# Kernel optimization log

Hardware: AMD Instinct MI355X
Metric: run time of the kernel (lower is better)

Reference implementation:

```python
import jax, jax.numpy as jnp
import numpy as np

NUM_HEADS = 8
ROPE_THETA = 10.0


def _axial_angles(height, width, head_dim, theta):
    # frequencies: 1/theta^(arange(0, head_dim, 4)[:head_dim//4] / head_dim)  -> [head_dim//4]
    hd4 = head_dim // 4
    freqs = 1.0 / (theta ** (np.arange(0, head_dim, 4)[:hd4].astype(np.float32) / head_dim))
    t = np.arange(height * width)
    t_x = (t % width).astype(np.float32)
    t_y = (t // width).astype(np.float32)
    ang_x = np.outer(t_x, freqs)  # [n, head_dim//4]
    ang_y = np.outer(t_y, freqs)
    return jnp.asarray(ang_x), jnp.asarray(ang_y)


def _apply_rope(x, cos, sin):
    # x: [b, h, n, half]; cos/sin: [n, half//2]; complex-pair rotation on last dim
    xr = x[..., 0::2]
    xi = x[..., 1::2]
    out_r = xr * cos - xi * sin
    out_i = xr * sin + xi * cos
    return jnp.stack([out_r, out_i], axis=-1).reshape(x.shape)


def setup_inputs() -> dict:
    key = jax.random.key(0)
    ks = jax.random.split(key, 5)
    b, n, c = 4, 16384, 512
    x = jax.random.normal(ks[0], (b, n, c), dtype=jnp.float32)
    w_qkv = jax.random.normal(ks[1], (c, 3 * c), dtype=jnp.float32) * 0.02
    b_qkv = jax.random.normal(ks[2], (3 * c,), dtype=jnp.float32) * 0.02
    w_proj = jax.random.normal(ks[3], (c, c), dtype=jnp.float32) * 0.02
    b_proj = jax.random.normal(ks[4], (c,), dtype=jnp.float32) * 0.02
    return {"x": x, "w_qkv": w_qkv, "b_qkv": b_qkv, "w_proj": w_proj, "b_proj": b_proj,
            "height": 128, "width": 128}


def reference(x, w_qkv, b_qkv, w_proj, b_proj, height, width):
    b, n, c = x.shape
    h = NUM_HEADS
    hd = c // h
    half = hd // 2

    qkv = (x @ w_qkv + b_qkv).reshape(b, n, 3, h, hd).transpose(2, 0, 3, 1, 4)
    q, k, v = qkv[0], qkv[1], qkv[2]  # each [b, h, n, hd]

    ang_x, ang_y = _axial_angles(height, width, hd, ROPE_THETA)
    cx, sx = jnp.cos(ang_x), jnp.sin(ang_x)
    cy, sy = jnp.cos(ang_y), jnp.sin(ang_y)

    q = jnp.concatenate([_apply_rope(q[..., :half], cx, sx),
                         _apply_rope(q[..., half:], cy, sy)], axis=-1)
    k = jnp.concatenate([_apply_rope(k[..., :half], cx, sx),
                         _apply_rope(k[..., half:], cy, sy)], axis=-1)

    # kernel feature map: elu(x) + 1 (positive)
    q = jax.nn.elu(q) + 1.0
    k = jax.nn.elu(k) + 1.0

    # linear attention: O(n d^2)
    kv = jnp.einsum('bhnd,bhne->bhde', k, v)
    out = jnp.einsum('bhnd,bhde->bhne', q, kv)
    z = 1.0 / (jnp.einsum('bhnd,bhd->bhn', q, k.sum(axis=2)) + 1e-6)
    out = out * z[..., None]

    out = out.transpose(0, 2, 1, 3).reshape(b, n, c)
    return out @ w_proj + b_proj
```

## Files before the change

kernel.cpp:

```cpp
#include <hip/hip_runtime.h>
#include <math.h>

#define BATCH 4
#define NTOK  16384
#define CDIM  512
#define NH    8
#define HD    64
#define M_ROWS (BATCH*NTOK)
#define KDIM  512

typedef _Float16 f16;
typedef _Float16 f16x8 __attribute__((ext_vector_type(8)));
typedef _Float16 f16x4 __attribute__((ext_vector_type(4)));
typedef _Float16 f16x2 __attribute__((ext_vector_type(2)));
typedef float    f32x4 __attribute__((ext_vector_type(4)));

__device__ __forceinline__ void load_lds16(const void* g, void* l) {
    __builtin_amdgcn_global_load_lds(
        (const __attribute__((address_space(1))) void*)g,
        (__attribute__((address_space(3))) void*)l, 16, 0, 0);
}

__global__ void rope_tables(float* __restrict__ tab) {
    int tid = threadIdx.x;
    for (int i = 0; i < 16; i++) {
        int idx = tid + i * 256;
        int t   = (idx >> 4) & 127;
        int fi  = idx & 15;
        double freq = pow(10.0, -(double)fi / 16.0);
        double ang  = (double)t * freq;
        tab[idx * 2]     = (float)cos(ang);
        tab[idx * 2 + 1] = (float)sin(ang);
    }
}

__global__ void convert_x_f16(const float* __restrict__ in, f16* __restrict__ outp) {
    int i = blockIdx.x * 256 + threadIdx.x;
    float4 a = *(const float4*)&in[(size_t)i * 8];
    float4 b = *(const float4*)&in[(size_t)i * 8 + 4];
    f16x8 o;
    o[0]=(f16)a.x; o[1]=(f16)a.y; o[2]=(f16)a.z; o[3]=(f16)a.w;
    o[4]=(f16)b.x; o[5]=(f16)b.y; o[6]=(f16)b.z; o[7]=(f16)b.w;
    *(f16x8*)&outp[(size_t)i * 8] = o;
}

template<int PERM>
__global__ void convert_wT(const float* __restrict__ w, f16* __restrict__ wt, int N) {
    int idx = blockIdx.x * 256 + threadIdx.x;
    int n = idx >> 9, k = idx & 511;
    int tc = n;
    if (PERM) {
        int blk = n >> 5, pos = n & 31;
        tc = blk * 32 + ((pos < 16) ? (pos * 2) : ((pos - 16) * 2 + 1));
    }
    wt[idx] = (f16)w[(size_t)k * N + tc];
}

template<int MODE>
__global__ __launch_bounds__(256, 2)
void gemm_f16(const f16* __restrict__ A, const f16* __restrict__ Bt,
              const float* __restrict__ bias,
              float* __restrict__ Co,
              f16* __restrict__ qd, f16* __restrict__ kd, f16* __restrict__ vd,
              const float* __restrict__ tab, int ncol_tiles)
{
    __shared__ f16 As[128 * 64];
    __shared__ f16 Bs[128 * 64];
    const int tid  = threadIdx.x;
    const int lane = tid & 63;
    const int wave = tid >> 6;
    const int wy = wave >> 1, wx = wave & 1;

    const int bid = blockIdx.x;
    const int xcd = bid & 7;
    const int idx = bid >> 3;
    const int ct  = idx % ncol_tiles;
    const int rt  = (idx / ncol_tiles) * 8 + xcd;
    const int row0 = rt * 128;
    const int col0 = ct * 128;

    const int l15 = lane & 15;
    const int l4  = lane >> 4;

    f32x4 acc[4][4];
    #pragma unroll
    for (int mt = 0; mt < 4; mt++)
        #pragma unroll
        for (int nt = 0; nt < 4; nt++)
            acc[mt][nt] = (f32x4){0.f, 0.f, 0.f, 0.f};

    const int pbase = wave * 256;

    for (int k0 = 0; k0 < KDIM; k0 += 64) {
        #pragma unroll
        for (int i = 0; i < 4; i++) {
            int p  = pbase + i * 64 + lane;
            int m  = p >> 3;
            int jp = p & 7;
            int j  = jp ^ (m & 7);
            load_lds16(&A [(size_t)(row0 + m) * KDIM + k0 + j * 8],
                       &As[(pbase + i * 64) * 8]);
            load_lds16(&Bt[(size_t)(col0 + m) * KDIM + k0 + j * 8],
                       &Bs[(pbase + i * 64) * 8]);
        }
        __syncthreads();

        #pragma unroll
        for (int s = 0; s < 2; s++) {
            f16x8 af[4], bf[4];
            #pragma unroll
            for (int t = 0; t < 4; t++) {
                int ra = wy * 64 + t * 16 + l15;
                int rb = wx * 64 + t * 16 + l15;
                int ca = ((s << 2) | l4) ^ (ra & 7);
                int cb = ((s << 2) | l4) ^ (rb & 7);
                af[t] = *(const f16x8*)&As[ra * 64 + ca * 8];
                bf[t] = *(const f16x8*)&Bs[rb * 64 + cb * 8];
            }
            #pragma unroll
            for (int mt = 0; mt < 4; mt++)
                #pragma unroll
                for (int nt = 0; nt < 4; nt++)
                    acc[mt][nt] = __builtin_amdgcn_mfma_f32_16x16x32_f16(af[mt], bf[nt], acc[mt][nt], 0, 0, 0);
        }
        __syncthreads();
    }

    if (MODE == 0) {
        float* ep = (float*)&As[0];
        #pragma unroll
        for (int mt = 0; mt < 4; mt++) {
            #pragma unroll
            for (int nt = 0; nt < 4; nt++) {
                int col = wx * 64 + nt * 16 + l15;
                float bv = bias[col0 + col];
                #pragma unroll
                for (int r = 0; r < 4; r++) {
                    int rp = wy * 16 + l4 * 4 + r;
                    ep[rp * 128 + col] = acc[mt][nt][r] + bv;
                }
            }
            __syncthreads();
            #pragma unroll
            for (int j = 0; j < 4; j++) {
                int id = tid + j * 256;
                int rp = id >> 5, c4 = id & 31;
                int grow = row0 + (rp >> 4) * 64 + mt * 16 + (rp & 15);
                float4 v4 = *(const float4*)&ep[rp * 128 + c4 * 4];
                *(float4*)&Co[(size_t)grow * CDIM + col0 + c4 * 4] = v4;
            }
            __syncthreads();
        }
    } else {
        const int which = col0 >> 9;
        f16* dst = (which == 0) ? qd : (which == 1) ? kd : vd;
        const float2* tab2 = (const float2*)tab;
        #pragma unroll
        for (int q = 0; q < 2; q++) {
            int B32  = (col0 + wx * 64 + q * 32) >> 5;
            int t0   = B32 * 32 + 2 * l15;
            int c512 = t0 & 511;
            float bv0 = bias[t0];
            float bv1 = bias[t0 + 1];
            int isy  = B32 & 1;
            const float2* ct = tab2 + isy * 2048 + l15;
            if (which == 2) {
                #pragma unroll
                for (int mt = 0; mt < 4; mt++)
                    #pragma unroll
                    for (int r = 0; r < 4; r++) {
                        int row = row0 + wy * 64 + mt * 16 + l4 * 4 + r;
                        f16x2 pk;
                        pk[0] = (f16)(acc[mt][2 * q][r]     + bv0);
                        pk[1] = (f16)(acc[mt][2 * q + 1][r] + bv1);
                        *(f16x2*)&dst[(size_t)row * CDIM + c512] = pk;
                    }
            } else {
                #pragma unroll
                for (int mt = 0; mt < 4; mt++)
                    #pragma unroll
                    for (int r = 0; r < 4; r++) {
                        int row = row0 + wy * 64 + mt * 16 + l4 * 4 + r;
                        int tok = row & (NTOK - 1);
                        int t   = isy ? (tok >> 7) : (tok & 127);
                        float2 cs = ct[t * 16];
                        float xr = acc[mt][2 * q][r]     + bv0;
                        float xi = acc[mt][2 * q + 1][r] + bv1;
                        float o_r = xr * cs.x - xi * cs.y;
                        float o_i = xr * cs.y + xi * cs.x;
                        o_r = (o_r > 0.f) ? o_r + 1.f : __expf(o_r);
                        o_i = (o_i > 0.f) ? o_i + 1.f : __expf(o_i);
                        f16x2 pk; pk[0] = (f16)o_r; pk[1] = (f16)o_i;
                        *(f16x2*)&dst[(size_t)row * CDIM + c512] = pk;
                    }
            }
        }
    }
}

__global__ __launch_bounds__(256, 4)
void kv_kernel(const f16* __restrict__ kk, const f16* __restrict__ vv,
               float* __restrict__ kvt, float* __restrict__ ksum)
{
    int bh = blockIdx.x;
    int b = bh >> 3, h = bh & 7;
    int t0 = blockIdx.y * 1024;
    __shared__ float ks[64][68];
    __shared__ float vs[64][68];
    int tid = threadIdx.x;
    int tx = tid & 15;
    int ty = tid >> 4;
    float acc[4][4];
    float ksacc[4];
    #pragma unroll
    for (int r = 0; r < 4; r++) { ksacc[r] = 0.f;
        #pragma unroll
        for (int j = 0; j < 4; j++) acc[r][j] = 0.f; }

    const size_t rowbase = (size_t)b * NTOK;
    for (int tt = t0; tt < t0 + 1024; tt += 64) {
        #pragma unroll
        for (int i = 0; i < 2; i++) {
            int idx = tid + i * 256;
            int tok = idx >> 3;
            int o   = (idx & 7) * 8;
            size_t g = (rowbase + tt + tok) * CDIM + h * HD + o;
            f16x8 k8 = *(const f16x8*)&kk[g];
            f16x8 v8 = *(const f16x8*)&vv[g];
            float4 klo = {(float)k8[0], (float)k8[1], (float)k8[2], (float)k8[3]};
            float4 khi = {(float)k8[4], (float)k8[5], (float)k8[6], (float)k8[7]};
            float4 vlo = {(float)v8[0], (float)v8[1], (float)v8[2], (float)v8[3]};
            float4 vhi = {(float)v8[4], (float)v8[5], (float)v8[6], (float)v8[7]};
            *(float4*)&ks[tok][o]     = klo;
            *(float4*)&ks[tok][o + 4] = khi;
            *(float4*)&vs[tok][o]     = vlo;
            *(float4*)&vs[tok][o + 4] = vhi;
        }
        __syncthreads();
        #pragma unroll 8
        for (int t = 0; t < 64; t++) {
            float4 kd4 = *(const float4*)&ks[t][ty * 4];
            float4 vd4 = *(const float4*)&vs[t][tx * 4];
            float ka[4] = {kd4.x, kd4.y, kd4.z, kd4.w};
            float va[4] = {vd4.x, vd4.y, vd4.z, vd4.w};
            #pragma unroll
            for (int r = 0; r < 4; r++) {
                ksacc[r] += ka[r];
                #pragma unroll
                for (int j = 0; j < 4; j++) acc[r][j] += ka[r] * va[j];
            }
        }
        __syncthreads();
    }
    #pragma unroll
    for (int r = 0; r < 4; r++)
        #pragma unroll
        for (int j = 0; j < 4; j++)
            atomicAdd(&kvt[bh * 4096 + (tx * 4 + j) * 64 + (ty * 4 + r)], acc[r][j]);
    if (tx == 0) {
        #pragma unroll
        for (int r = 0; r < 4; r++) atomicAdd(&ksum[bh * 64 + ty * 4 + r], ksacc[r]);
    }
}

__global__ __launch_bounds__(256, 4)
void attn_kernel(const f16* __restrict__ q, const float* __restrict__ kvt,
                 const float* __restrict__ ksum, f16* __restrict__ attnh)
{
    int bh = blockIdx.x;
    int b = bh >> 3, h = bh & 7;
    int rc = blockIdx.y;
    __shared__ f16 kvhi[64 * 64];
    __shared__ f16 kvlo[64 * 64];
    int tid = threadIdx.x;
    const int lane = tid & 63;
    const int wave = tid >> 6;
    const int l15 = lane & 15;
    const int l4  = lane >> 4;

    {
        int e = tid >> 2;
        #pragma unroll
        for (int c = 0; c < 2; c++) {
            int chunk = (tid & 3) * 2 + c;
            f16x8 hi8, lo8;
            #pragma unroll
            for (int j = 0; j < 8; j++) {
                float v = kvt[bh * 4096 + e * 64 + chunk * 8 + j];
                f16 hv = (f16)v;
                hi8[j] = hv;
                lo8[j] = (f16)(v - (float)hv);
            }
            int cp = chunk ^ (e & 7);
            *(f16x8*)&kvhi[e * 64 + cp * 8] = hi8;
            *(f16x8*)&kvlo[e * 64 + cp * 8] = lo8;
        }
    }
    float ksA[2][8];
    #pragma unroll
    for (int s = 0; s < 2; s++)
        #pragma unroll
        for (int j = 0; j < 8; j++)
            ksA[s][j] = ksum[bh * 64 + s * 32 + l4 * 8 + j];
    __syncthreads();

    f16x8 bhi[2][4], blo[2][4];
    #pragma unroll
    for (int s = 0; s < 2; s++)
        #pragma unroll
        for (int nt = 0; nt < 4; nt++) {
            int e  = nt * 16 + l15;
            int cp = ((s << 2) | l4) ^ (e & 7);
            bhi[s][nt] = *(const f16x8*)&kvhi[e * 64 + cp * 8];
            blo[s][nt] = *(const f16x8*)&kvlo[e * 64 + cp * 8];
        }

    const size_t qbase = ((size_t)b * NTOK + rc * 256 + wave * 64) * CDIM + (size_t)h * HD;

    #pragma unroll
    for (int mt = 0; mt < 4; mt++) {
        f16x8 af[2];
        #pragma unroll
        for (int s = 0; s < 2; s++)
            af[s] = *(const f16x8*)&q[qbase + (size_t)(mt * 16 + l15) * CDIM + s * 32 + l4 * 8];

        float zp = 0.f;
        #pragma unroll
        for (int s = 0; s < 2; s++)
            #pragma unroll
            for (int j = 0; j < 8; j++)
                zp += (float)af[s][j] * ksA[s][j];
        zp += __shfl_xor(zp, 16, 64);
        zp += __shfl_xor(zp, 32, 64);
        float zinv = 1.f / (zp + 1e-6f);

        f32x4 acc[4];
        #pragma unroll
        for (int nt = 0; nt < 4; nt++) acc[nt] = (f32x4){0.f, 0.f, 0.f, 0.f};
        #pragma unroll
        for (int s = 0; s < 2; s++)
            #pragma unroll
            for (int nt = 0; nt < 4; nt++) {
                acc[nt] = __builtin_amdgcn_mfma_f32_16x16x32_f16(af[s], bhi[s][nt], acc[nt], 0, 0, 0);
                acc[nt] = __builtin_amdgcn_mfma_f32_16x16x32_f16(af[s], blo[s][nt], acc[nt], 0, 0, 0);
            }

        #pragma unroll
        for (int r = 0; r < 4; r++) {
            float zr = __shfl(zinv, l4 * 4 + r, 64);
            size_t orow = qbase + (size_t)(mt * 16 + l4 * 4 + r) * CDIM;
            #pragma unroll
            for (int nt = 0; nt < 4; nt++)
                attnh[orow + nt * 16 + l15] = (f16)(acc[nt][r] * zr);
        }
    }
}

extern "C" void kernel_launch(void* const* d_in, const int* in_sizes, int n_in,
                              void* d_out, int out_size, void* d_ws, size_t ws_size,
                              hipStream_t stream)
{
    const float* x      = (const float*)d_in[0];
    const float* w_qkv  = (const float*)d_in[1];
    const float* b_qkv  = (const float*)d_in[2];
    const float* w_proj = (const float*)d_in[3];
    const float* b_proj = (const float*)d_in[4];
    float* out = (float*)d_out;
    char*  ws  = (char*)d_ws;

    const size_t NCB = (size_t)M_ROWS * CDIM * sizeof(f16);
    f16*   xh   = (f16*)(ws);
    f16*   qh   = (f16*)(ws + NCB * 1);
    f16*   kh   = (f16*)(ws + NCB * 2);
    f16*   vh   = (f16*)(ws + NCB * 3);
    f16*   wqt  = (f16*)(ws + NCB * 4);
    f16*   wpt  = (f16*)(ws + NCB * 4 + (1536 * 512) * sizeof(f16));
    float* tab  = (float*)(ws + NCB * 4 + (1536 * 512 + 512 * 512) * sizeof(f16));
    float* kvp  = tab + 8192;
    float* ksum = kvp + 32 * 4096;

    hipMemsetAsync(kvp, 0, (32 * 4096 + 32 * 64) * sizeof(float), stream);
    rope_tables<<<1, 256, 0, stream>>>(tab);
    convert_x_f16<<<M_ROWS * CDIM / 8 / 256, 256, 0, stream>>>(x, xh);
    convert_wT<1><<<1536 * 512 / 256, 256, 0, stream>>>(w_qkv, wqt, 1536);
    convert_wT<0><<<512 * 512 / 256, 256, 0, stream>>>(w_proj, wpt, 512);

    gemm_f16<1><<<6144, 256, 0, stream>>>(xh, wqt, b_qkv,
                                          nullptr, qh, kh, vh, tab, 12);
    kv_kernel<<<dim3(32, 16), 256, 0, stream>>>(kh, vh, kvp, ksum);
    attn_kernel<<<dim3(32, 64), 256, 0, stream>>>(qh, kvp, ksum, vh);
    gemm_f16<0><<<2048, 256, 0, stream>>>(vh, wpt, b_proj,
                                          out, nullptr, nullptr, nullptr, nullptr, 4);
}
```

Measured before the change: 548.6 us.

## Restructure kv reduction, split kv packing kernel, and write GEMM output directly

The projection GEMM epilogue now writes biased results straight from registers as float2 stores, replacing the LDS-staged coalesced float4 path; the w_proj conversion switches to the permuted (mode 1) layout to match. kv_kernel gives each wave its own token slice with an 8x8 register tile per thread, reduces the four waves through LDS, and issues far fewer global atomics. A new kv_pack kernel converts kv to hi/lo f16 once, so attn_kernel loads it directly instead of converting and staging in LDS in every block. The cost is an extra launch, less coalesced output stores, and higher register pressure in kv_kernel.

Result: no change. 537.9 us (-1.9%).

```diff
diff --git a/kernel.cpp b/kernel.cpp
--- a/kernel.cpp
+++ b/kernel.cpp
@@ -127,29 +127,22 @@
     }
 
     if (MODE == 0) {
-        float* ep = (float*)&As[0];
-        #pragma unroll
-        for (int mt = 0; mt < 4; mt++) {
-            #pragma unroll
-            for (int nt = 0; nt < 4; nt++) {
-                int col = wx * 64 + nt * 16 + l15;
-                float bv = bias[col0 + col];
+        #pragma unroll
+        for (int q = 0; q < 2; q++) {
+            int B32 = (col0 + wx * 64 + q * 32) >> 5;
+            int t0c = B32 * 32 + 2 * l15;
+            float bv0 = bias[t0c];
+            float bv1 = bias[t0c + 1];
+            #pragma unroll
+            for (int mt = 0; mt < 4; mt++)
                 #pragma unroll
                 for (int r = 0; r < 4; r++) {
-                    int rp = wy * 16 + l4 * 4 + r;
-                    ep[rp * 128 + col] = acc[mt][nt][r] + bv;
+                    int row = row0 + wy * 64 + mt * 16 + l4 * 4 + r;
+                    float2 o2;
+                    o2.x = acc[mt][2 * q][r]     + bv0;
+                    o2.y = acc[mt][2 * q + 1][r] + bv1;
+                    *(float2*)&Co[(size_t)row * CDIM + t0c] = o2;
                 }
-            }
-            __syncthreads();
-            #pragma unroll
-            for (int j = 0; j < 4; j++) {
-                int id = tid + j * 256;
-                int rp = id >> 5, c4 = id & 31;
-                int grow = row0 + (rp >> 4) * 64 + mt * 16 + (rp & 15);
-                float4 v4 = *(const float4*)&ep[rp * 128 + c4 * 4];
-                *(float4*)&Co[(size_t)grow * CDIM + col0 + c4 * 4] = v4;
-            }
-            __syncthreads();
         }
     } else {
         const int which = col0 >> 9;
@@ -208,14 +201,18 @@
     __shared__ float ks[64][68];
     __shared__ float vs[64][68];
     int tid = threadIdx.x;
-    int tx = tid & 15;
-    int ty = tid >> 4;
-    float acc[4][4];
-    float ksacc[4];
-    #pragma unroll
-    for (int r = 0; r < 4; r++) { ksacc[r] = 0.f;
-        #pragma unroll
-        for (int j = 0; j < 4; j++) acc[r][j] = 0.f; }
+    const int wave = tid >> 6;
+    const int lane = tid & 63;
+    const int ly = lane >> 3;
+    const int lx = lane & 7;
+    const int o  = (tid & 7) * 8;
+
+    float acc[8][8];
+    float ksacc[8];
+    #pragma unroll
+    for (int r = 0; r < 8; r++) { ksacc[r] = 0.f;
+        #pragma unroll
+        for (int j = 0; j < 8; j++) acc[r][j] = 0.f; }
 
     const size_t rowbase = (size_t)b * NTOK;
     for (int tt = t0; tt < t0 + 1024; tt += 64) {
@@ -223,7 +220,6 @@
         for (int i = 0; i < 2; i++) {
             int idx = tid + i * 256;
             int tok = idx >> 3;
-            int o   = (idx & 7) * 8;
             size_t g = (rowbase + tt + tok) * CDIM + h * HD + o;
             f16x8 k8 = *(const f16x8*)&kk[g];
             f16x8 v8 = *(const f16x8*)&vv[g];
@@ -235,85 +231,116 @@
             *(float4*)&ks[tok][o + 4] = khi;
             *(float4*)&vs[tok][o]     = vlo;
             *(float4*)&vs[tok][o + 4] = vhi;
+            ksacc[0] += klo.x; ksacc[1] += klo.y; ksacc[2] += klo.z; ksacc[3] += klo.w;
+            ksacc[4] += khi.x; ksacc[5] += khi.y; ksacc[6] += khi.z; ksacc[7] += khi.w;
         }
         __syncthreads();
-        #pragma unroll 8
-        for (int t = 0; t < 64; t++) {
-            float4 kd4 = *(const float4*)&ks[t][ty * 4];
-            float4 vd4 = *(const float4*)&vs[t][tx * 4];
-            float ka[4] = {kd4.x, kd4.y, kd4.z, kd4.w};
-            float va[4] = {vd4.x, vd4.y, vd4.z, vd4.w};
-            #pragma unroll
-            for (int r = 0; r < 4; r++) {
-                ksacc[r] += ka[r];
+        #pragma unroll
+        for (int t5 = 0; t5 < 16; t5++) {
+            int t = wave * 16 + t5;
+            float4 ka0 = *(const float4*)&ks[t][ly * 8];
+            float4 ka1 = *(const float4*)&ks[t][ly * 8 + 4];
+            float4 va0 = *(const float4*)&vs[t][lx * 8];
+            float4 va1 = *(const float4*)&vs[t][lx * 8 + 4];
+            float ka[8] = {ka0.x, ka0.y, ka0.z, ka0.w, ka1.x, ka1.y, ka1.z, ka1.w};
+            float va[8] = {va0.x, va0.y, va0.z, va0.w, va1.x, va1.y, va1.z, va1.w};
+            #pragma unroll
+            for (int r = 0; r < 8; r++)
                 #pragma unroll
-                for (int j = 0; j < 4; j++) acc[r][j] += ka[r] * va[j];
+                for (int j = 0; j < 8; j++) acc[r][j] += ka[r] * va[j];
+        }
+        __syncthreads();
+    }
+
+    float* ksl = &vs[0][0];
+    {
+        float4 a = {ksacc[0], ksacc[1], ksacc[2], ksacc[3]};
+        float4 c = {ksacc[4], ksacc[5], ksacc[6], ksacc[7]};
+        *(float4*)&ksl[tid * 8]     = a;
+        *(float4*)&ksl[tid * 8 + 4] = c;
+    }
+    float* red = &ks[0][0];
+    #pragma unroll
+    for (int w = 0; w < 4; w++) {
+        if (wave == w) {
+            #pragma unroll
+            for (int j = 0; j < 8; j++) {
+                int base = (lx * 8 + j) * 64 + ly * 8;
+                float4 lo = {acc[0][j], acc[1][j], acc[2][j], acc[3][j]};
+                float4 hi = {acc[4][j], acc[5][j], acc[6][j], acc[7][j]};
+                if (w == 0) {
+                    *(float4*)&red[base]     = lo;
+                    *(float4*)&red[base + 4] = hi;
+                } else {
+                    float4 p0 = *(const float4*)&red[base];
+                    float4 p1 = *(const float4*)&red[base + 4];
+                    p0.x += lo.x; p0.y += lo.y; p0.z += lo.z; p0.w += lo.w;
+                    p1.x += hi.x; p1.y += hi.y; p1.z += hi.z; p1.w += hi.w;
+                    *(float4*)&red[base]     = p0;
+                    *(float4*)&red[base + 4] = p1;
+                }
             }
         }
         __syncthreads();
     }
     #pragma unroll
-    for (int r = 0; r < 4; r++)
-        #pragma unroll
-        for (int j = 0; j < 4; j++)
-            atomicAdd(&kvt[bh * 4096 + (tx * 4 + j) * 64 + (ty * 4 + r)], acc[r][j]);
-    if (tx == 0) {
-        #pragma unroll
-        for (int r = 0; r < 4; r++) atomicAdd(&ksum[bh * 64 + ty * 4 + r], ksacc[r]);
-    }
+    for (int i = 0; i < 16; i++) {
+        int idx = tid + i * 256;
+        atomicAdd(&kvt[bh * 4096 + idx], red[idx]);
+    }
+    if (tid < 64) {
+        float s = 0.f;
+        #pragma unroll
+        for (int m = 0; m < 32; m++)
+            s += ksl[((tid >> 3) + m * 8) * 8 + (tid & 7)];
+        atomicAdd(&ksum[bh * 64 + tid], s);
+    }
+}
+
+__global__ void kv_pack(const float* __restrict__ kvt,
+                        f16* __restrict__ kvhi, f16* __restrict__ kvlo)
+{
+    int idx = blockIdx.x * 256 + threadIdx.x;
+    float4 v = *(const float4*)&kvt[idx * 4];
+    f16x4 hi, lo;
+    hi[0] = (f16)v.x; lo[0] = (f16)(v.x - (float)hi[0]);
+    hi[1] = (f16)v.y; lo[1] = (f16)(v.y - (float)hi[1]);
+    hi[2] = (f16)v.z; lo[2] = (f16)(v.z - (float)hi[2]);
+    hi[3] = (f16)v.w; lo[3] = (f16)(v.w - (float)hi[3]);
+    *(f16x4*)&kvhi[idx * 4] = hi;
+    *(f16x4*)&kvlo[idx * 4] = lo;
 }
 
 __global__ __launch_bounds__(256, 4)
-void attn_kernel(const f16* __restrict__ q, const float* __restrict__ kvt,
-                 const float* __restrict__ ksum, f16* __restrict__ attnh)
+void attn_kernel(const f16* __restrict__ q, const f16* __restrict__ kvhi,
+                 const f16* __restrict__ kvlo, const float* __restrict__ ksum,
+                 f16* __restrict__ attnh)
 {
     int bh = blockIdx.x;
     int b = bh >> 3, h = bh & 7;
     int rc = blockIdx.y;
-    __shared__ f16 kvhi[64 * 64];
-    __shared__ f16 kvlo[64 * 64];
     int tid = threadIdx.x;
     const int lane = tid & 63;
     const int wave = tid >> 6;
     const int l15 = lane & 15;
     const int l4  = lane >> 4;
 
-    {
-        int e = tid >> 2;
-        #pragma unroll
-        for (int c = 0; c < 2; c++) {
-            int chunk = (tid & 3) * 2 + c;
-            f16x8 hi8, lo8;
-            #pragma unroll
-            for (int j = 0; j < 8; j++) {
-                float v = kvt[bh * 4096 + e * 64 + chunk * 8 + j];
-                f16 hv = (f16)v;
-                hi8[j] = hv;
-                lo8[j] = (f16)(v - (float)hv);
-            }
-            int cp = chunk ^ (e & 7);
-            *(f16x8*)&kvhi[e * 64 + cp * 8] = hi8;
-            *(f16x8*)&kvlo[e * 64 + cp * 8] = lo8;
-        }
-    }
+    f16x8 bhi[2][4], blo[2][4];
+    #pragma unroll
+    for (int s = 0; s < 2; s++)
+        #pragma unroll
+        for (int nt = 0; nt < 4; nt++) {
+            int e = nt * 16 + l15;
+            size_t gb = (size_t)bh * 4096 + e * 64 + s * 32 + l4 * 8;
+            bhi[s][nt] = *(const f16x8*)&kvhi[gb];
+            blo[s][nt] = *(const f16x8*)&kvlo[gb];
+        }
     float ksA[2][8];
     #pragma unroll
     for (int s = 0; s < 2; s++)
         #pragma unroll
         for (int j = 0; j < 8; j++)
             ksA[s][j] = ksum[bh * 64 + s * 32 + l4 * 8 + j];
-    __syncthreads();
-
-    f16x8 bhi[2][4], blo[2][4];
-    #pragma unroll
-    for (int s = 0; s < 2; s++)
-        #pragma unroll
-        for (int nt = 0; nt < 4; nt++) {
-            int e  = nt * 16 + l15;
-            int cp = ((s << 2) | l4) ^ (e & 7);
-            bhi[s][nt] = *(const f16x8*)&kvhi[e * 64 + cp * 8];
-            blo[s][nt] = *(const f16x8*)&kvlo[e * 64 + cp * 8];
-        }
 
     const size_t qbase = ((size_t)b * NTOK + rc * 256 + wave * 64) * CDIM + (size_t)h * HD;
 
@@ -378,17 +405,20 @@
     float* tab  = (float*)(ws + NCB * 4 + (1536 * 512 + 512 * 512) * sizeof(f16));
     float* kvp  = tab + 8192;
     float* ksum = kvp + 32 * 4096;
+    f16*   kvhi = (f16*)(ksum + 32 * 64);
+    f16*   kvlo = kvhi + 32 * 4096;
 
     hipMemsetAsync(kvp, 0, (32 * 4096 + 32 * 64) * sizeof(float), stream);
     rope_tables<<<1, 256, 0, stream>>>(tab);
     convert_x_f16<<<M_ROWS * CDIM / 8 / 256, 256, 0, stream>>>(x, xh);
     convert_wT<1><<<1536 * 512 / 256, 256, 0, stream>>>(w_qkv, wqt, 1536);
-    convert_wT<0><<<512 * 512 / 256, 256, 0, stream>>>(w_proj, wpt, 512);
+    convert_wT<1><<<512 * 512 / 256, 256, 0, stream>>>(w_proj, wpt, 512);
 
     gemm_f16<1><<<6144, 256, 0, stream>>>(xh, wqt, b_qkv,
                                           nullptr, qh, kh, vh, tab, 12);
     kv_kernel<<<dim3(32, 16), 256, 0, stream>>>(kh, vh, kvp, ksum);
-    attn_kernel<<<dim3(32, 64), 256, 0, stream>>>(qh, kvp, ksum, vh);
+    kv_pack<<<128, 256, 0, stream>>>(kvp, kvhi, kvlo);
+    attn_kernel<<<dim3(32, 64), 256, 0, stream>>>(qh, kvhi, kvlo, ksum, vh);
     gemm_f16<0><<<2048, 256, 0, stream>>>(vh, wpt, b_proj,
                                           out, nullptr, nullptr, nullptr, nullptr, 4);
 }
```
